# Performance work log

Measured on AMD Instinct MI355X. Metric: run time of the kernel, lower is better.

The kernel has to match this reference:

```python
import jax, jax.numpy as jnp
import numpy as np

N = 10000          # nodes
E = 160000         # edges (avg degree 16)
F = 240            # invariant features_dim
H_INV, D_INV = 4, 60    # invariant heads / head dim
H_EV, D_EV = 3, 80      # equivariant heads (= len(degrees)) / head dim
RBF = 32
DEGREES = [1, 2, 3]
REPEATS = np.array([2 * l + 1 for l in DEGREES])   # [3,5,7]
EV_DIM = int(REPEATS.sum())                        # 15
OFFS = np.concatenate([[0], np.cumsum(REPEATS)])   # [0,3,8,15]


def _kaiming_uniform(key, shape, fan_in):
    # torch kaiming_uniform_ with a=sqrt(5): bound = 1/sqrt(fan_in)
    b = 1.0 / np.sqrt(fan_in)
    return jax.random.uniform(key, shape, minval=-b, maxval=b, dtype=jnp.float32)


def setup_inputs() -> dict:
    key = jax.random.key(0)
    ks = jax.random.split(key, 16)
    return {
        "inv_features": jax.random.normal(ks[0], (N, F), dtype=jnp.float32),
        "ev_features": jax.random.normal(ks[1], (N, EV_DIM), dtype=jnp.float32),
        "rbf": jax.random.uniform(ks[2], (E, RBF), dtype=jnp.float32),
        "sh_vectors": jax.random.normal(ks[3], (E, EV_DIM), dtype=jnp.float32),
        "cutoffs": jax.random.uniform(ks[4], (E, 1), dtype=jnp.float32),
        "W_q_inv": _kaiming_uniform(ks[5], (H_INV, D_INV, D_INV), D_INV),
        "W_k_inv": _kaiming_uniform(ks[6], (H_INV, D_INV, D_INV), D_INV),
        "W_v_inv": _kaiming_uniform(ks[7], (H_INV, D_INV, D_INV), D_INV),
        "W_q_ev": _kaiming_uniform(ks[8], (H_EV, D_EV, D_EV), D_EV),
        "W_k_ev": _kaiming_uniform(ks[9], (H_EV, D_EV, D_EV), D_EV),
        "W_filt_inv": _kaiming_uniform(ks[10], (RBF + len(DEGREES), F), RBF + len(DEGREES)),
        "b_filt_inv": jnp.zeros((F,), dtype=jnp.float32),
        "W_filt_ev": _kaiming_uniform(ks[11], (RBF + len(DEGREES), F), RBF + len(DEGREES)),
        "b_filt_ev": jnp.zeros((F,), dtype=jnp.float32),
        "senders": jax.random.randint(ks[12], (E,), 0, N, dtype=jnp.int32),
        "receivers": jax.random.randint(ks[13], (E,), 0, N, dtype=jnp.int32),
    }


def reference(inv_features, ev_features, rbf, sh_vectors, cutoffs,
              W_q_inv, W_k_inv, W_v_inv, W_q_ev, W_k_ev,
              W_filt_inv, b_filt_inv, W_filt_ev, b_filt_ev,
              senders, receivers):
    n = inv_features.shape[0]
    # edge-wise equivariant differences [E, 15]
    ev_diff = ev_features[senders] - ev_features[receivers]
    # per-degree SO3 invariants: sum over m components of each degree -> [E, 3]
    invs = jnp.stack([(ev_diff[:, OFFS[i]:OFFS[i + 1]] ** 2).sum(-1)
                      for i in range(len(DEGREES))], axis=-1)
    f_in = jnp.concatenate([rbf, invs], axis=-1)           # [E, RBF+3]
    fw_inv = (f_in @ W_filt_inv + b_filt_inv).reshape(-1, H_INV, D_INV)
    fw_ev = (f_in @ W_filt_ev + b_filt_ev).reshape(-1, H_EV, D_EV)

    xi = inv_features.reshape(-1, H_INV, D_INV)
    xe = inv_features.reshape(-1, H_EV, D_EV)
    q_inv = jnp.einsum('hij,nhi->nhj', W_q_inv, xi)[receivers]
    k_inv = jnp.einsum('hij,nhi->nhj', W_k_inv, xi)[senders]
    v_inv = jnp.einsum('hij,nhi->nhj', W_v_inv, xi)[senders]
    q_ev = jnp.einsum('hij,nhi->nhj', W_q_ev, xe)[receivers]
    k_ev = jnp.einsum('hij,nhi->nhj', W_k_ev, xe)[senders]

    alpha_inv = (q_inv * (k_inv * fw_inv)).sum(-1, keepdims=True) / np.sqrt(D_INV)  # [E,H,1]
    alpha_ev = (q_ev * (k_ev * fw_ev)).sum(-1) / np.sqrt(D_EV)                      # [E,3]

    scaled_inv = cutoffs[:, None] * alpha_inv * v_inv       # [E,H,D]
    d_inv = jax.ops.segment_sum(scaled_inv, receivers, num_segments=n).reshape(n, -1)

    alpha_ev_r = jnp.repeat(alpha_ev, REPEATS, axis=-1, total_repeat_length=EV_DIM)  # [E,15]
    scaled_ev = cutoffs * alpha_ev_r * sh_vectors
    d_ev = jax.ops.segment_sum(scaled_ev, receivers, num_segments=n)
    return d_inv, d_ev
```

## Files before the change

### kernel.cpp

```cpp
#include <hip/hip_runtime.h>

#define PNPB 32

__global__ __launch_bounds__(512) void proj_kernel(
    const float* __restrict__ x,
    const float* __restrict__ Wq, const float* __restrict__ Wk,
    const float* __restrict__ Wv,
    const float* __restrict__ Wqe, const float* __restrict__ Wke,
    float* __restrict__ q_inv, float* __restrict__ k_inv,
    float* __restrict__ v_inv,
    float* __restrict__ q_ev, float* __restrict__ k_ev, int N)
{
    __shared__ float xs[PNPB * 240];
    const int base_node = blockIdx.x * PNPB;
    for (int idx = threadIdx.x; idx < PNPB * 240; idx += 512) {
        int g = base_node * 240 + idx;
        xs[idx] = (g < N * 240) ? x[g] : 0.f;
    }
    __syncthreads();

    const int slot = threadIdx.x & 63;
    const int wg   = threadIdx.x >> 6;
    if (slot >= 60) return;

    const int hi  = slot / 15;
    const int jdi = slot * 4 - hi * 60;
    const int he  = slot / 20;
    const int jde = slot * 4 - he * 80;
    const int nl0 = wg * 4;

    float4 aq[4], ak[4], av[4], aqe[4], ake[4];
    #pragma unroll
    for (int n = 0; n < 4; ++n) {
        aq[n] = make_float4(0.f,0.f,0.f,0.f); ak[n] = aq[n]; av[n] = aq[n];
        aqe[n] = aq[n]; ake[n] = aq[n];
    }
    {
        const float* wq = Wq + hi * 3600 + jdi;
        const float* wk = Wk + hi * 3600 + jdi;
        const float* wv = Wv + hi * 3600 + jdi;
        const float* xb = &xs[nl0 * 240 + hi * 60];
        #pragma unroll 2
        for (int i = 0; i < 60; ++i) {
            float xv0 = xb[i], xv1 = xb[240 + i], xv2 = xb[480 + i], xv3 = xb[720 + i];
            float4 w;
            w = *(const float4*)&wq[i * 60];
            aq[0].x += xv0*w.x; aq[0].y += xv0*w.y; aq[0].z += xv0*w.z; aq[0].w += xv0*w.w;
            aq[1].x += xv1*w.x; aq[1].y += xv1*w.y; aq[1].z += xv1*w.z; aq[1].w += xv1*w.w;
            aq[2].x += xv2*w.x; aq[2].y += xv2*w.y; aq[2].z += xv2*w.z; aq[2].w += xv2*w.w;
            aq[3].x += xv3*w.x; aq[3].y += xv3*w.y; aq[3].z += xv3*w.z; aq[3].w += xv3*w.w;
            w = *(const float4*)&wk[i * 60];
            ak[0].x += xv0*w.x; ak[0].y += xv0*w.y; ak[0].z += xv0*w.z; ak[0].w += xv0*w.w;
            ak[1].x += xv1*w.x; ak[1].y += xv1*w.y; ak[1].z += xv1*w.z; ak[1].w += xv1*w.w;
            ak[2].x += xv2*w.x; ak[2].y += xv2*w.y; ak[2].z += xv2*w.z; ak[2].w += xv2*w.w;
            ak[3].x += xv3*w.x; ak[3].y += xv3*w.y; ak[3].z += xv3*w.z; ak[3].w += xv3*w.w;
            w = *(const float4*)&wv[i * 60];
            av[0].x += xv0*w.x; av[0].y += xv0*w.y; av[0].z += xv0*w.z; av[0].w += xv0*w.w;
            av[1].x += xv1*w.x; av[1].y += xv1*w.y; av[1].z += xv1*w.z; av[1].w += xv1*w.w;
            av[2].x += xv2*w.x; av[2].y += xv2*w.y; av[2].z += xv2*w.z; av[2].w += xv2*w.w;
            av[3].x += xv3*w.x; av[3].y += xv3*w.y; av[3].z += xv3*w.z; av[3].w += xv3*w.w;
        }
    }
    {
        const float* wq = Wqe + he * 6400 + jde;
        const float* wk = Wke + he * 6400 + jde;
        const float* xb = &xs[nl0 * 240 + he * 80];
        #pragma unroll 2
        for (int i = 0; i < 80; ++i) {
            float xv0 = xb[i], xv1 = xb[240 + i], xv2 = xb[480 + i], xv3 = xb[720 + i];
            float4 w;
            w = *(const float4*)&wq[i * 80];
            aqe[0].x += xv0*w.x; aqe[0].y += xv0*w.y; aqe[0].z += xv0*w.z; aqe[0].w += xv0*w.w;
            aqe[1].x += xv1*w.x; aqe[1].y += xv1*w.y; aqe[1].z += xv1*w.z; aqe[1].w += xv1*w.w;
            aqe[2].x += xv2*w.x; aqe[2].y += xv2*w.y; aqe[2].z += xv2*w.z; aqe[2].w += xv2*w.w;
            aqe[3].x += xv3*w.x; aqe[3].y += xv3*w.y; aqe[3].z += xv3*w.z; aqe[3].w += xv3*w.w;
            w = *(const float4*)&wk[i * 80];
            ake[0].x += xv0*w.x; ake[0].y += xv0*w.y; ake[0].z += xv0*w.z; ake[0].w += xv0*w.w;
            ake[1].x += xv1*w.x; ake[1].y += xv1*w.y; ake[1].z += xv1*w.z; ake[1].w += xv1*w.w;
            ake[2].x += xv2*w.x; ake[2].y += xv2*w.y; ake[2].z += xv2*w.z; ake[2].w += xv2*w.w;
            ake[3].x += xv3*w.x; ake[3].y += xv3*w.y; ake[3].z += xv3*w.z; ake[3].w += xv3*w.w;
        }
    }
    #pragma unroll
    for (int n = 0; n < 4; ++n) {
        const int node = base_node + nl0 + n;
        if (node >= N) break;
        const int ob = node * 240 + slot * 4;
        *(float4*)&q_inv[ob] = aq[n];
        *(float4*)&k_inv[ob] = ak[n];
        *(float4*)&v_inv[ob] = av[n];
        *(float4*)&q_ev[ob]  = aqe[n];
        *(float4*)&k_ev[ob]  = ake[n];
    }
}

__global__ __launch_bounds__(256) void hist_kernel(
    const int* __restrict__ rcv, int* __restrict__ counts, int E)
{
    int e = blockIdx.x * 256 + threadIdx.x;
    if (e < E) atomicAdd(&counts[rcv[e]], 1);
}

__global__ __launch_bounds__(1024) void scan_kernel(
    const int* __restrict__ counts, int* __restrict__ rowstart,
    int* __restrict__ cursor, int N)
{
    __shared__ int wsum[16];
    __shared__ int carry_s;
    if (threadIdx.x == 0) carry_s = 0;
    __syncthreads();
    const int lane = threadIdx.x & 63;
    const int w    = threadIdx.x >> 6;
    for (int base = 0; base < N; base += 1024) {
        const int i = base + threadIdx.x;
        int v = (i < N) ? counts[i] : 0;
        int x = v;
        #pragma unroll
        for (int off = 1; off < 64; off <<= 1) {
            int t = __shfl_up(x, off);
            if (lane >= off) x += t;
        }
        if (lane == 63) wsum[w] = x;
        __syncthreads();
        if (w == 0) {
            int s = (lane < 16) ? wsum[lane] : 0;
            #pragma unroll
            for (int off = 1; off < 16; off <<= 1) {
                int t = __shfl_up(s, off);
                if (lane >= off) s += t;
            }
            if (lane < 16) wsum[lane] = s;
        }
        __syncthreads();
        const int woff = (w == 0) ? 0 : wsum[w - 1];
        const int ex = carry_s + woff + x - v;
        if (i < N) { rowstart[i] = ex; cursor[i] = ex; }
        __syncthreads();
        if (threadIdx.x == 1023) carry_s += wsum[15];
    }
    __syncthreads();
    if (threadIdx.x == 0) rowstart[N] = carry_s;
}

__global__ __launch_bounds__(256) void scatter_kernel(
    const int* __restrict__ rcv, int* __restrict__ cursor,
    int* __restrict__ csr, int E)
{
    int e = blockIdx.x * 256 + threadIdx.x;
    if (e < E) {
        int pos = atomicAdd(&cursor[rcv[e]], 1);
        csr[pos] = e;
    }
}

__global__ __launch_bounds__(256) void inv3_kernel(
    const float* __restrict__ ev_f, const int* __restrict__ snd,
    const int* __restrict__ rcv, float* __restrict__ inv3, int E)
{
    int e = blockIdx.x * 256 + threadIdx.x;
    if (e >= E) return;
    const float* es = ev_f + (size_t)snd[e] * 15;
    const float* er = ev_f + (size_t)rcv[e] * 15;
    float i0 = 0.f, i1 = 0.f, i2 = 0.f;
    #pragma unroll
    for (int q = 0; q < 3; ++q)  { float d = es[q] - er[q]; i0 = fmaf(d, d, i0); }
    #pragma unroll
    for (int q = 3; q < 8; ++q)  { float d = es[q] - er[q]; i1 = fmaf(d, d, i1); }
    #pragma unroll
    for (int q = 8; q < 15; ++q) { float d = es[q] - er[q]; i2 = fmaf(d, d, i2); }
    *(float4*)(inv3 + (size_t)e * 4) = make_float4(i0, i1, i2, 0.f);
}

__global__ __launch_bounds__(128) void alpha_fused_kernel(
    const float* __restrict__ rbf, const float* __restrict__ inv3,
    const float* __restrict__ cut,
    const float* __restrict__ Wfi, const float* __restrict__ bfi,
    const float* __restrict__ Wfe, const float* __restrict__ bfe,
    const int* __restrict__ snd,   const int* __restrict__ rcv,
    const float* __restrict__ q_inv, const float* __restrict__ k_inv,
    const float* __restrict__ q_ev,  const float* __restrict__ k_ev,
    float* __restrict__ alpha, int E)
{
    __shared__ float WS[35 * 240];
    __shared__ float BS[240];
    const int part = blockIdx.y;
    {
        const float* Wsrc = part ? Wfe : Wfi;
        const float* bsrc = part ? bfe : bfi;
        for (int idx = threadIdx.x; idx < 35 * 240; idx += 128)
            WS[idx] = Wsrc[idx];
        for (int idx = threadIdx.x; idx < 240; idx += 128)
            BS[idx] = bsrc[idx];
    }
    __syncthreads();

    const int base = blockIdx.x * 256;
    int e0 = base + threadIdx.x;
    int e1 = base + 128 + threadIdx.x;
    if (e0 >= E) e0 = E - 1;
    if (e1 >= E) e1 = E - 1;

    const int s0 = snd[e0], r0 = rcv[e0];
    const int s1 = snd[e1], r1 = rcv[e1];
    const float c0 = cut[e0], c1 = cut[e1];

    float f0[35], f1[35];
    {
        const float4* rb0 = (const float4*)(rbf + (size_t)e0 * 32);
        const float4* rb1 = (const float4*)(rbf + (size_t)e1 * 32);
        #pragma unroll
        for (int k4 = 0; k4 < 8; ++k4) {
            float4 a = rb0[k4], b = rb1[k4];
            f0[k4*4+0] = a.x; f0[k4*4+1] = a.y; f0[k4*4+2] = a.z; f0[k4*4+3] = a.w;
            f1[k4*4+0] = b.x; f1[k4*4+1] = b.y; f1[k4*4+2] = b.z; f1[k4*4+3] = b.w;
        }
        float4 v0 = *(const float4*)(inv3 + (size_t)e0 * 4);
        float4 v1 = *(const float4*)(inv3 + (size_t)e1 * 4);
        f0[32] = v0.x; f0[33] = v0.y; f0[34] = v0.z;
        f1[32] = v1.x; f1[33] = v1.y; f1[34] = v1.z;
    }

    if (part == 0) {
        const float s60 = 0.12909944487358056f;
        const float* q0b = q_inv + (size_t)r0 * 240;
        const float* k0b = k_inv + (size_t)s0 * 240;
        const float* q1b = q_inv + (size_t)r1 * 240;
        const float* k1b = k_inv + (size_t)s1 * 240;
        #pragma unroll
        for (int h = 0; h < 4; ++h) {
            float acc0 = 0.f, acc1 = 0.f;
            #pragma unroll 1
            for (int j4 = 0; j4 < 15; ++j4) {
                const int j = h * 60 + j4 * 4;
                const float4 b4 = *(const float4*)&BS[j];
                float4 fw0 = b4, fw1 = b4;
                #pragma unroll
                for (int k = 0; k < 35; ++k) {
                    const float4 w = *(const float4*)&WS[k * 240 + j];
                    const float a0 = f0[k], a1 = f1[k];
                    fw0.x = fmaf(a0, w.x, fw0.x); fw0.y = fmaf(a0, w.y, fw0.y);
                    fw0.z = fmaf(a0, w.z, fw0.z); fw0.w = fmaf(a0, w.w, fw0.w);
                    fw1.x = fmaf(a1, w.x, fw1.x); fw1.y = fmaf(a1, w.y, fw1.y);
                    fw1.z = fmaf(a1, w.z, fw1.z); fw1.w = fmaf(a1, w.w, fw1.w);
                }
                float4 q, kk;
                q  = *(const float4*)(q0b + j);
                kk = *(const float4*)(k0b + j);
                acc0 += q.x*kk.x*fw0.x + q.y*kk.y*fw0.y
                      + q.z*kk.z*fw0.z + q.w*kk.w*fw0.w;
                q  = *(const float4*)(q1b + j);
                kk = *(const float4*)(k1b + j);
                acc1 += q.x*kk.x*fw1.x + q.y*kk.y*fw1.y
                      + q.z*kk.z*fw1.z + q.w*kk.w*fw1.w;
            }
            alpha[(size_t)e0 * 8 + h] = acc0 * s60 * c0;
            alpha[(size_t)e1 * 8 + h] = acc1 * s60 * c1;
        }
        alpha[(size_t)e0 * 8 + 7] = __int_as_float(s0);
        alpha[(size_t)e1 * 8 + 7] = __int_as_float(s1);
    } else {
        const float s80 = 0.11180339887498948f;
        const float* q0b = q_ev + (size_t)r0 * 240;
        const float* k0b = k_ev + (size_t)s0 * 240;
        const float* q1b = q_ev + (size_t)r1 * 240;
        const float* k1b = k_ev + (size_t)s1 * 240;
        #pragma unroll
        for (int h = 0; h < 3; ++h) {
            float acc0 = 0.f, acc1 = 0.f;
            #pragma unroll 1
            for (int j4 = 0; j4 < 20; ++j4) {
                const int j = h * 80 + j4 * 4;
                const float4 b4 = *(const float4*)&BS[j];
                float4 fw0 = b4, fw1 = b4;
                #pragma unroll
                for (int k = 0; k < 35; ++k) {
                    const float4 w = *(const float4*)&WS[k * 240 + j];
                    const float a0 = f0[k], a1 = f1[k];
                    fw0.x = fmaf(a0, w.x, fw0.x); fw0.y = fmaf(a0, w.y, fw0.y);
                    fw0.z = fmaf(a0, w.z, fw0.z); fw0.w = fmaf(a0, w.w, fw0.w);
                    fw1.x = fmaf(a1, w.x, fw1.x); fw1.y = fmaf(a1, w.y, fw1.y);
                    fw1.z = fmaf(a1, w.z, fw1.z); fw1.w = fmaf(a1, w.w, fw1.w);
                }
                float4 q, kk;
                q  = *(const float4*)(q0b + j);
                kk = *(const float4*)(k0b + j);
                acc0 += q.x*kk.x*fw0.x + q.y*kk.y*fw0.y
                      + q.z*kk.z*fw0.z + q.w*kk.w*fw0.w;
                q  = *(const float4*)(q1b + j);
                kk = *(const float4*)(k1b + j);
                acc1 += q.x*kk.x*fw1.x + q.y*kk.y*fw1.y
                      + q.z*kk.z*fw1.z + q.w*kk.w*fw1.w;
            }
            alpha[(size_t)e0 * 8 + 4 + h] = acc0 * s80 * c0;
            alpha[(size_t)e1 * 8 + 4 + h] = acc1 * s80 * c1;
        }
    }
}

__global__ __launch_bounds__(256) void gather_kernel(
    const int* __restrict__ rowstart, const int* __restrict__ csr,
    const float* __restrict__ alpha,
    const float* __restrict__ v_inv, const float* __restrict__ sh,
    float* __restrict__ dinv, float* __restrict__ dev)
{
    const int r = blockIdx.x;
    const int c = threadIdx.x;
    const int beg = rowstart[r], end = rowstart[r + 1];

    __shared__ float sal[64][8];
    __shared__ int   sed[64];

    float acc = 0.f;
    for (int chunk = beg; chunk < end; chunk += 64) {
        const int len = min(64, end - chunk);
        __syncthreads();
        if (c < len) {
            const int ed = csr[chunk + c];
            sed[c] = ed;
            const float4* ap = (const float4*)(alpha + (size_t)ed * 8);
            const float4 a0 = ap[0], a1 = ap[1];
            *(float4*)&sal[c][0] = a0;
            *(float4*)&sal[c][4] = a1;
        }
        __syncthreads();
        if (c < 240) {
            const int h = c / 60;
            #pragma unroll 4
            for (int i = 0; i < len; ++i) {
                const int s = __float_as_int(sal[i][7]);
                acc += sal[i][h] * v_inv[(size_t)s * 240 + c];
            }
        } else if (c < 255) {
            const int i0 = c - 240;
            const int h = (i0 < 3) ? 4 : ((i0 < 8) ? 5 : 6);
            for (int i = 0; i < len; ++i)
                acc += sal[i][h] * sh[(size_t)sed[i] * 15 + i0];
        }
    }
    if (c < 240) dinv[(size_t)r * 240 + c] = acc;
    else if (c < 255) dev[(size_t)r * 15 + (c - 240)] = acc;
}

extern "C" void kernel_launch(void* const* d_in, const int* in_sizes, int n_in,
                              void* d_out, int out_size, void* d_ws, size_t ws_size,
                              hipStream_t stream) {
    const float* inv_f = (const float*)d_in[0];
    const float* ev_f  = (const float*)d_in[1];
    const float* rbf   = (const float*)d_in[2];
    const float* sh    = (const float*)d_in[3];
    const float* cut   = (const float*)d_in[4];
    const float* Wq    = (const float*)d_in[5];
    const float* Wk    = (const float*)d_in[6];
    const float* Wv    = (const float*)d_in[7];
    const float* Wqe   = (const float*)d_in[8];
    const float* Wke   = (const float*)d_in[9];
    const float* Wfi   = (const float*)d_in[10];
    const float* bfi   = (const float*)d_in[11];
    const float* Wfe   = (const float*)d_in[12];
    const float* bfe   = (const float*)d_in[13];
    const int*   snd   = (const int*)d_in[14];
    const int*   rcv   = (const int*)d_in[15];

    const int N = in_sizes[0] / 240;
    const int E = in_sizes[14];

    float* out  = (float*)d_out;
    float* dinv = out;
    float* dev  = out + (size_t)N * 240;

    float* ws = (float*)d_ws;
    const size_t Nf = (size_t)N * 240;
    float* q_inv = ws + 0 * Nf;
    float* k_inv = ws + 1 * Nf;
    float* v_inv = ws + 2 * Nf;
    float* q_ev  = ws + 3 * Nf;
    float* k_ev  = ws + 4 * Nf;
    float* alpha = ws + 5 * Nf;
    float* inv3  = alpha + (size_t)E * 8;
    int*   ibase    = (int*)(inv3 + (size_t)E * 4);
    int*   counts   = ibase;
    int*   rowstart = ibase + N;
    int*   cursor   = ibase + 2 * N + 1;
    int*   csr      = ibase + 3 * N + 1;

    hipMemsetAsync(counts, 0, (size_t)N * sizeof(int), stream);

    const int eb = (E + 255) / 256;
    hist_kernel<<<eb, 256, 0, stream>>>(rcv, counts, E);
    scan_kernel<<<1, 1024, 0, stream>>>(counts, rowstart, cursor, N);
    scatter_kernel<<<eb, 256, 0, stream>>>(rcv, cursor, csr, E);

    proj_kernel<<<(N + PNPB - 1) / PNPB, 512, 0, stream>>>(
        inv_f, Wq, Wk, Wv, Wqe, Wke, q_inv, k_inv, v_inv, q_ev, k_ev, N);

    inv3_kernel<<<eb, 256, 0, stream>>>(ev_f, snd, rcv, inv3, E);

    const int ab = (E + 255) / 256;
    alpha_fused_kernel<<<dim3(ab, 2), 128, 0, stream>>>(
        rbf, inv3, cut, Wfi, bfi, Wfe, bfe, snd, rcv,
        q_inv, k_inv, q_ev, k_ev, alpha, E);

    gather_kernel<<<N, 256, 0, stream>>>(
        rowstart, csr, alpha, v_inv, sh, dinv, dev);
}
```

Baseline: 436.5 us.

## Compute alpha in CSR (receiver-sorted) order and enlarge alpha blocks

The alpha kernel now walks edges in CSR order via csr[i] and writes alpha at the CSR position, so gather reads alpha contiguously instead of through an indirect index. Receiver-sorted edges also make q lookups repeat the same rows, which should improve cache reuse. Block size is raised to 256 threads with a 3-blocks-per-SM occupancy hint, which halves how often the weight table is staged into shared memory relative to the edges processed. It adds one indirect csr load per edge, and the launch-bounds hint may force register spilling given the 70-float per-thread arrays.

```diff
diff --git a/kernel.cpp b/kernel.cpp
--- a/kernel.cpp
+++ b/kernel.cpp
@@ -171,12 +171,13 @@
     *(float4*)(inv3 + (size_t)e * 4) = make_float4(i0, i1, i2, 0.f);
 }
 
-__global__ __launch_bounds__(128) void alpha_fused_kernel(
+__global__ __launch_bounds__(256, 3) void alpha_fused_kernel(
     const float* __restrict__ rbf, const float* __restrict__ inv3,
     const float* __restrict__ cut,
     const float* __restrict__ Wfi, const float* __restrict__ bfi,
     const float* __restrict__ Wfe, const float* __restrict__ bfe,
     const int* __restrict__ snd,   const int* __restrict__ rcv,
+    const int* __restrict__ csr,
     const float* __restrict__ q_inv, const float* __restrict__ k_inv,
     const float* __restrict__ q_ev,  const float* __restrict__ k_ev,
     float* __restrict__ alpha, int E)
@@ -187,18 +188,20 @@
     {
         const float* Wsrc = part ? Wfe : Wfi;
         const float* bsrc = part ? bfe : bfi;
-        for (int idx = threadIdx.x; idx < 35 * 240; idx += 128)
+        for (int idx = threadIdx.x; idx < 35 * 240; idx += 256)
             WS[idx] = Wsrc[idx];
-        for (int idx = threadIdx.x; idx < 240; idx += 128)
+        for (int idx = threadIdx.x; idx < 240; idx += 256)
             BS[idx] = bsrc[idx];
     }
     __syncthreads();
 
-    const int base = blockIdx.x * 256;
-    int e0 = base + threadIdx.x;
-    int e1 = base + 128 + threadIdx.x;
-    if (e0 >= E) e0 = E - 1;
-    if (e1 >= E) e1 = E - 1;
+    const int base = blockIdx.x * 512;
+    int i0 = base + threadIdx.x;
+    int i1 = base + 256 + threadIdx.x;
+    if (i0 >= E) i0 = E - 1;
+    if (i1 >= E) i1 = E - 1;
+    const int e0 = csr[i0];
+    const int e1 = csr[i1];
 
     const int s0 = snd[e0], r0 = rcv[e0];
     const int s1 = snd[e1], r1 = rcv[e1];
@@ -219,6 +222,8 @@
         f0[32] = v0.x; f0[33] = v0.y; f0[34] = v0.z;
         f1[32] = v1.x; f1[33] = v1.y; f1[34] = v1.z;
     }
+
+    float out0[8], out1[8];
 
     if (part == 0) {
         const float s60 = 0.12909944487358056f;
@@ -253,11 +258,15 @@
                 acc1 += q.x*kk.x*fw1.x + q.y*kk.y*fw1.y
                       + q.z*kk.z*fw1.z + q.w*kk.w*fw1.w;
             }
-            alpha[(size_t)e0 * 8 + h] = acc0 * s60 * c0;
-            alpha[(size_t)e1 * 8 + h] = acc1 * s60 * c1;
-        }
-        alpha[(size_t)e0 * 8 + 7] = __int_as_float(s0);
-        alpha[(size_t)e1 * 8 + 7] = __int_as_float(s1);
+            out0[h] = acc0 * s60 * c0;
+            out1[h] = acc1 * s60 * c1;
+        }
+        out0[7] = __int_as_float(s0);
+        out1[7] = __int_as_float(s1);
+        *(float4*)(alpha + (size_t)i0 * 8) = make_float4(out0[0], out0[1], out0[2], out0[3]);
+        *(float4*)(alpha + (size_t)i1 * 8) = make_float4(out1[0], out1[1], out1[2], out1[3]);
+        alpha[(size_t)i0 * 8 + 7] = out0[7];
+        alpha[(size_t)i1 * 8 + 7] = out1[7];
     } else {
         const float s80 = 0.11180339887498948f;
         const float* q0b = q_ev + (size_t)r0 * 240;
@@ -291,9 +300,15 @@
                 acc1 += q.x*kk.x*fw1.x + q.y*kk.y*fw1.y
                       + q.z*kk.z*fw1.z + q.w*kk.w*fw1.w;
             }
-            alpha[(size_t)e0 * 8 + 4 + h] = acc0 * s80 * c0;
-            alpha[(size_t)e1 * 8 + 4 + h] = acc1 * s80 * c1;
-        }
+            out0[4 + h] = acc0 * s80 * c0;
+            out1[4 + h] = acc1 * s80 * c1;
+        }
+        alpha[(size_t)i0 * 8 + 4] = out0[4];
+        alpha[(size_t)i0 * 8 + 5] = out0[5];
+        alpha[(size_t)i0 * 8 + 6] = out0[6];
+        alpha[(size_t)i1 * 8 + 4] = out1[4];
+        alpha[(size_t)i1 * 8 + 5] = out1[5];
+        alpha[(size_t)i1 * 8 + 6] = out1[6];
     }
 }
 
@@ -315,12 +330,11 @@
         const int len = min(64, end - chunk);
         __syncthreads();
         if (c < len) {
-            const int ed = csr[chunk + c];
-            sed[c] = ed;
-            const float4* ap = (const float4*)(alpha + (size_t)ed * 8);
+            const float4* ap = (const float4*)(alpha + (size_t)(chunk + c) * 8);
             const float4 a0 = ap[0], a1 = ap[1];
             *(float4*)&sal[c][0] = a0;
             *(float4*)&sal[c][4] = a1;
+            sed[c] = csr[chunk + c];
         }
         __syncthreads();
         if (c < 240) {
@@ -395,9 +409,9 @@
 
     inv3_kernel<<<eb, 256, 0, stream>>>(ev_f, snd, rcv, inv3, E);
 
-    const int ab = (E + 255) / 256;
-    alpha_fused_kernel<<<dim3(ab, 2), 128, 0, stream>>>(
-        rbf, inv3, cut, Wfi, bfi, Wfe, bfe, snd, rcv,
+    const int ab = (E + 511) / 512;
+    alpha_fused_kernel<<<dim3(ab, 2), 256, 0, stream>>>(
+        rbf, inv3, cut, Wfi, bfi, Wfe, bfe, snd, rcv, csr,
         q_inv, k_inv, q_ev, k_ev, alpha, E);
 
     gather_kernel<<<N, 256, 0, stream>>>(
```

Measured after the change: 391.9 us. 1.11x faster.
